# Optimization experiments

Hardware: AMD Instinct MI355X
Metric: run time of the kernel (lower is better)

## Reference

```python
import jax, jax.numpy as jnp
import numpy as np

N_NODES = 100000
N_EDGES = 1600000


def _gcn_conv(x, src, dst, W, b, n_nodes):
    """PyG GCNConv: add self-loops, symmetric norm, linear, scatter-add."""
    h = x @ W  # [N, out]
    # append self-loops
    loop = jnp.arange(n_nodes, dtype=src.dtype)
    s = jnp.concatenate([src, loop])
    d = jnp.concatenate([dst, loop])
    # degree over destinations (with self-loops)
    deg = jax.ops.segment_sum(jnp.ones_like(d, dtype=h.dtype), d, num_segments=n_nodes)
    dinv = jax.lax.rsqrt(jnp.maximum(deg, 1.0))
    norm = dinv[s] * dinv[d]  # [E+N]
    msg = h[s] * norm[:, None]  # [E+N, out] gather + scale
    out = jax.ops.segment_sum(msg, d, num_segments=n_nodes)  # scatter-add
    return out + b


def setup_inputs() -> dict:
    key = jax.random.key(0)
    k1, k2, k3, k4 = jax.random.split(key, 4)
    x = jax.random.normal(k1, (N_NODES, 10), dtype=jnp.float32)
    edge_index = jax.random.randint(k2, (2, N_EDGES), 0, N_NODES, dtype=jnp.int64)
    W1 = jax.random.normal(k3, (10, 64), dtype=jnp.float32) * (1.0 / np.sqrt(10))
    b1 = jnp.zeros((64,), dtype=jnp.float32)
    W2 = jax.random.normal(k4, (64, 10), dtype=jnp.float32) * (1.0 / np.sqrt(64))
    b2 = jnp.zeros((10,), dtype=jnp.float32)
    return {"x": x, "edge_index": edge_index, "W1": W1, "b1": b1, "W2": W2, "b2": b2}


def reference(x, edge_index, W1, b1, W2, b2):
    src, dst = edge_index[0], edge_index[1]
    h = _gcn_conv(x, src, dst, W1, b1, N_NODES)
    h = jax.nn.relu(h)
    # dropout is identity in eval mode
    h = _gcn_conv(h, src, dst, W2, b2, N_NODES)
    return jax.nn.log_softmax(h, axis=1)
```

## Files before the change

### kernel.cpp

```cpp
#include <hip/hip_runtime.h>
#include <hip/hip_fp16.h>

#define N_NODES 100000
#define N_EDGES 1600000

#define NPB   256
#define NB    391
#define PCAP  8192
#define ABLK  256
#define ATHR  1024
#define CAP   64

typedef unsigned int u32;

__device__ __forceinline__ float2 h2f2(u32 u) {
    __half2 h = *reinterpret_cast<__half2*>(&u);
    return __half22float2(h);
}

__global__ void zero_tail_kernel(int* __restrict__ tail) {
    tail[threadIdx.x] = 0;
}

__global__ __launch_bounds__(ATHR) void bucket_kernel(
    const int* __restrict__ src, const int* __restrict__ dst,
    int* __restrict__ tail, int* __restrict__ pairs, int E) {
    __shared__ int lcnt[NB];
    __shared__ int bbase[NB];
    const int tid = threadIdx.x;
    for (int b = tid; b < NB; b += ATHR) lcnt[b] = 0;
    __syncthreads();

    const int chunk = (E + gridDim.x - 1) / gridDim.x;
    const int e0 = blockIdx.x * chunk;
    const int e1 = min(e0 + chunk, E);

    for (int e = e0 + tid; e < e1; e += ATHR)
        atomicAdd(&lcnt[dst[e] >> 8], 1);
    __syncthreads();

    for (int b = tid; b < NB; b += ATHR) {
        int n = lcnt[b];
        int ng8 = (n + 7) & ~7;
        int base = 0;
        if (ng8) {
            base = atomicAdd(&tail[b], ng8);
            if (base + ng8 <= PCAP) {
                for (int j = n; j < ng8; ++j) pairs[b * PCAP + base + j] = -1;
            }
        }
        bbase[b] = base;
        lcnt[b] = 0;
    }
    __syncthreads();

    for (int e = e0 + tid; e < e1; e += ATHR) {
        int d = dst[e];
        int b = d >> 8;
        int p = (src[e] << 8) | (d & 255);
        int pos = atomicAdd(&lcnt[b], 1);
        int idx = bbase[b] + pos;
        if (idx < PCAP) pairs[b * PCAP + idx] = p;
    }
}

__global__ __launch_bounds__(1024) void csr_kernel(
    const int* __restrict__ tail, const int* __restrict__ pairs,
    const float* __restrict__ x, int* __restrict__ cnt, int* __restrict__ slist,
    float* __restrict__ dinv, u32* __restrict__ xh, u32* __restrict__ th, int N) {
    __shared__ int ofs[NPB];
    const int b = blockIdx.x, tid = threadIdx.x;
    if (tid < NPB) ofs[tid] = 0;
    __syncthreads();
    const int n = min(tail[b], PCAP);
    const int* pb = pairs + b * PCAP;
    const int node0 = b * NPB;
    for (int i = tid; i < n; i += 1024) {
        int p = pb[i];
        if (p >= 0) {
            int dl = p & 255;
            int pos = atomicAdd(&ofs[dl], 1);
            if (pos < CAP) slist[(size_t)(node0 + dl) * CAP + pos] = p >> 8;
        }
    }
    __syncthreads();
    if (tid < NPB) {
        int node = node0 + tid;
        if (node < N) {
            int deg = min(ofs[tid], CAP);
            cnt[node] = deg;
            int padded = (deg + 3) & ~3;
            for (int j = deg; j < padded; ++j) slist[(size_t)node * CAP + j] = N_NODES;
            float di = rsqrtf((float)deg + 1.0f);
            dinv[node] = di;
            u32 h[8];
#pragma unroll
            for (int k = 0; k < 5; ++k) {
                __half2 hh = __floats2half2_rn(x[(size_t)node * 10 + 2 * k] * di,
                                               x[(size_t)node * 10 + 2 * k + 1] * di);
                h[k] = *reinterpret_cast<u32*>(&hh);
            }
            h[5] = h[6] = h[7] = 0u;
            u32* row = xh + (size_t)node * 8;
            ((uint4*)row)[0] = make_uint4(h[0], h[1], h[2], h[3]);
            ((uint4*)row)[1] = make_uint4(h[4], h[5], h[6], h[7]);
        }
    }
    if (b == 0 && tid == 0) {
        u32* rx = xh + (size_t)N * 8;
        u32* rt = th + (size_t)N * 8;
        ((uint4*)rx)[0] = make_uint4(0, 0, 0, 0); ((uint4*)rx)[1] = make_uint4(0, 0, 0, 0);
        ((uint4*)rt)[0] = make_uint4(0, 0, 0, 0); ((uint4*)rt)[1] = make_uint4(0, 0, 0, 0);
    }
}

__global__ void aggh_kernel(const u32* __restrict__ vh, const int* __restrict__ cnt,
                            const int* __restrict__ slist, float* __restrict__ out12, int N) {
    int gt = blockIdx.x * blockDim.x + threadIdx.x;
    int i = gt >> 1, cg = gt & 1;
    if (i >= N) return;
    int degi = cnt[i];
    const int* lst = slist + (size_t)i * CAP;
    float a[8];
    {
        uint4 s = *(((const uint4*)(vh + (size_t)i * 8)) + cg);
        float2 f0 = h2f2(s.x), f1 = h2f2(s.y), f2 = h2f2(s.z), f3 = h2f2(s.w);
        a[0] = f0.x; a[1] = f0.y; a[2] = f1.x; a[3] = f1.y;
        a[4] = f2.x; a[5] = f2.y; a[6] = f3.x; a[7] = f3.y;
    }
    for (int k = 0; k < degi; k += 4) {
        int4 s4 = *reinterpret_cast<const int4*>(lst + k);
        uint4 q0 = *(((const uint4*)(vh + (size_t)s4.x * 8)) + cg);
        uint4 q1 = *(((const uint4*)(vh + (size_t)s4.y * 8)) + cg);
        uint4 q2 = *(((const uint4*)(vh + (size_t)s4.z * 8)) + cg);
        uint4 q3 = *(((const uint4*)(vh + (size_t)s4.w * 8)) + cg);
        float2 f;
        f = h2f2(q0.x); a[0] += f.x; a[1] += f.y;  f = h2f2(q0.y); a[2] += f.x; a[3] += f.y;
        f = h2f2(q0.z); a[4] += f.x; a[5] += f.y;  f = h2f2(q0.w); a[6] += f.x; a[7] += f.y;
        f = h2f2(q1.x); a[0] += f.x; a[1] += f.y;  f = h2f2(q1.y); a[2] += f.x; a[3] += f.y;
        f = h2f2(q1.z); a[4] += f.x; a[5] += f.y;  f = h2f2(q1.w); a[6] += f.x; a[7] += f.y;
        f = h2f2(q2.x); a[0] += f.x; a[1] += f.y;  f = h2f2(q2.y); a[2] += f.x; a[3] += f.y;
        f = h2f2(q2.z); a[4] += f.x; a[5] += f.y;  f = h2f2(q2.w); a[6] += f.x; a[7] += f.y;
        f = h2f2(q3.x); a[0] += f.x; a[1] += f.y;  f = h2f2(q3.y); a[2] += f.x; a[3] += f.y;
        f = h2f2(q3.z); a[4] += f.x; a[5] += f.y;  f = h2f2(q3.w); a[6] += f.x; a[7] += f.y;
    }
    float* orow = out12 + (size_t)i * 12;
    if (cg == 0) {
        ((float4*)orow)[0] = make_float4(a[0], a[1], a[2], a[3]);
        ((float4*)orow)[1] = make_float4(a[4], a[5], a[6], a[7]);
    } else {
        *(float2*)(orow + 8) = make_float2(a[0], a[1]);
    }
}

__global__ void layer12_kernel(const float* __restrict__ agg12, const float* __restrict__ dinv,
                               const float* __restrict__ W1, const float* __restrict__ b1,
                               const float* __restrict__ W2, u32* __restrict__ th, int N) {
    __shared__ float sW1[640];
    __shared__ float sW2[640];
    __shared__ float sb1[64];
    for (int k = threadIdx.x; k < 640; k += blockDim.x) { sW1[k] = W1[k]; sW2[k] = W2[k]; }
    if (threadIdx.x < 64) sb1[threadIdx.x] = b1[threadIdx.x];
    __syncthreads();
    int i = blockIdx.x * blockDim.x + threadIdx.x;
    if (i >= N) return;
    float di = dinv[i];
    float ax[10];
#pragma unroll
    for (int k = 0; k < 10; ++k) ax[k] = di * agg12[(size_t)i * 12 + k];
    float o[10];
#pragma unroll
    for (int k = 0; k < 10; ++k) o[k] = 0.f;
    for (int c = 0; c < 64; ++c) {
        float y = sb1[c];
#pragma unroll
        for (int k = 0; k < 10; ++k) y = fmaf(ax[k], sW1[k * 64 + c], y);
        y = fmaxf(y, 0.f);
#pragma unroll
        for (int k = 0; k < 10; ++k) o[k] = fmaf(y, sW2[c * 10 + k], o[k]);
    }
    u32 h[8];
#pragma unroll
    for (int k = 0; k < 5; ++k) {
        __half2 hh = __floats2half2_rn(o[2 * k] * di, o[2 * k + 1] * di);
        h[k] = *reinterpret_cast<u32*>(&hh);
    }
    h[5] = h[6] = h[7] = 0u;
    u32* row = th + (size_t)i * 8;
    ((uint4*)row)[0] = make_uint4(h[0], h[1], h[2], h[3]);
    ((uint4*)row)[1] = make_uint4(h[4], h[5], h[6], h[7]);
}

__global__ void aggout_kernel(const u32* __restrict__ vh, const int* __restrict__ cnt,
                              const int* __restrict__ slist, const float* __restrict__ dinv,
                              const float* __restrict__ b2, float* __restrict__ out, int N) {
    int gt = blockIdx.x * blockDim.x + threadIdx.x;
    int i = gt >> 1, cg = gt & 1;
    bool valid = (i < N);
    float a[8];
#pragma unroll
    for (int k = 0; k < 8; ++k) a[k] = 0.f;
    if (valid) {
        int degi = cnt[i];
        const int* lst = slist + (size_t)i * CAP;
        {
            uint4 s = *(((const uint4*)(vh + (size_t)i * 8)) + cg);
            float2 f0 = h2f2(s.x), f1 = h2f2(s.y), f2 = h2f2(s.z), f3 = h2f2(s.w);
            a[0] = f0.x; a[1] = f0.y; a[2] = f1.x; a[3] = f1.y;
            a[4] = f2.x; a[5] = f2.y; a[6] = f3.x; a[7] = f3.y;
        }
        for (int k = 0; k < degi; k += 4) {
            int4 s4 = *reinterpret_cast<const int4*>(lst + k);
            uint4 q0 = *(((const uint4*)(vh + (size_t)s4.x * 8)) + cg);
            uint4 q1 = *(((const uint4*)(vh + (size_t)s4.y * 8)) + cg);
            uint4 q2 = *(((const uint4*)(vh + (size_t)s4.z * 8)) + cg);
            uint4 q3 = *(((const uint4*)(vh + (size_t)s4.w * 8)) + cg);
            float2 f;
            f = h2f2(q0.x); a[0] += f.x; a[1] += f.y;  f = h2f2(q0.y); a[2] += f.x; a[3] += f.y;
            f = h2f2(q0.z); a[4] += f.x; a[5] += f.y;  f = h2f2(q0.w); a[6] += f.x; a[7] += f.y;
            f = h2f2(q1.x); a[0] += f.x; a[1] += f.y;  f = h2f2(q1.y); a[2] += f.x; a[3] += f.y;
            f = h2f2(q1.z); a[4] += f.x; a[5] += f.y;  f = h2f2(q1.w); a[6] += f.x; a[7] += f.y;
            f = h2f2(q2.x); a[0] += f.x; a[1] += f.y;  f = h2f2(q2.y); a[2] += f.x; a[3] += f.y;
            f = h2f2(q2.z); a[4] += f.x; a[5] += f.y;  f = h2f2(q2.w); a[6] += f.x; a[7] += f.y;
            f = h2f2(q3.x); a[0] += f.x; a[1] += f.y;  f = h2f2(q3.y); a[2] += f.x; a[3] += f.y;
            f = h2f2(q3.z); a[4] += f.x; a[5] += f.y;  f = h2f2(q3.w); a[6] += f.x; a[7] += f.y;
        }
    }
    float v8 = __shfl_xor(a[0], 1);
    float v9 = __shfl_xor(a[1], 1);
    if (valid && cg == 0) {
        float di = dinv[i];
        float v[10] = { a[0], a[1], a[2], a[3], a[4], a[5], a[6], a[7], v8, v9 };
        float m = -1e30f;
#pragma unroll
        for (int c = 0; c < 10; ++c) {
            v[c] = fmaf(di, v[c], b2[c]);
            m = fmaxf(m, v[c]);
        }
        float s = 0.f;
#pragma unroll
        for (int c = 0; c < 10; ++c) s += __expf(v[c] - m);
        float lse = __logf(s) + m;
        float2* po = (float2*)(out + (size_t)i * 10);
#pragma unroll
        for (int c = 0; c < 5; ++c) po[c] = make_float2(v[2 * c] - lse, v[2 * c + 1] - lse);
    }
}

extern "C" void kernel_launch(void* const* d_in, const int* in_sizes, int n_in,
                              void* d_out, int out_size, void* d_ws, size_t ws_size,
                              hipStream_t stream) {
    const float* x  = (const float*)d_in[0];
    const int*   ei = (const int*)d_in[1];
    const float* W1 = (const float*)d_in[2];
    const float* b1 = (const float*)d_in[3];
    const float* W2 = (const float*)d_in[4];
    const float* b2 = (const float*)d_in[5];
    float* out = (float*)d_out;

    const int N = N_NODES, E = N_EDGES;
    const int* src = ei;
    const int* dst = ei + E;

    int*   tail  = (int*)d_ws;
    int*   pairs = tail + 512;
    int*   cnt   = pairs + (size_t)NB * PCAP;
    int*   slist = cnt + N;
    float* dinv  = (float*)(slist + (size_t)N * CAP);
    u32*   xh    = (u32*)(dinv + N);
    u32*   th    = xh + (size_t)(N + 1) * 8;
    float* agg12 = (float*)(th + (size_t)(N + 1) * 8);

    zero_tail_kernel<<<1, 512, 0, stream>>>(tail);
    bucket_kernel<<<ABLK, ATHR, 0, stream>>>(src, dst, tail, pairs, E);
    csr_kernel<<<NB, 1024, 0, stream>>>(tail, pairs, x, cnt, slist, dinv, xh, th, N);
    aggh_kernel<<<(2 * N + 255) / 256, 256, 0, stream>>>(xh, cnt, slist, agg12, N);
    layer12_kernel<<<(N + 255) / 256, 256, 0, stream>>>(agg12, dinv, W1, b1, W2, th, N);
    aggout_kernel<<<(2 * N + 255) / 256, 256, 0, stream>>>(th, cnt, slist, dinv, b2, out, N);
}
```

Baseline: 93.27 us.

## Use per-block fixed bucket slots and fuse aggregation with MLP layer

The bucketing pass now writes edges into fixed per-(bucket, block) slots with a count table. This removes the global tail atomics, the zeroing kernel and the second counting pass over the edge list. The first aggregation is fused with the dense two-layer MLP: the two threads per node exchange partial sums via shuffles and each computes half of the 64 hidden channels, which avoids the agg12 round-trip and one launch. The cost is that the CSR kernel now scans a fixed 256x64 slot grid per bucket. Slots are capped at 64 edges per block and bucket, so overflow would silently drop edges.

```diff
diff --git a/kernel.cpp b/kernel.cpp
--- a/kernel.cpp
+++ b/kernel.cpp
@@ -6,9 +6,9 @@
 
 #define NPB   256
 #define NB    391
-#define PCAP  8192
 #define ABLK  256
 #define ATHR  1024
+#define BSLOT 64
 #define CAP   64
 
 typedef unsigned int u32;
@@ -18,66 +18,47 @@
     return __half22float2(h);
 }
 
-__global__ void zero_tail_kernel(int* __restrict__ tail) {
-    tail[threadIdx.x] = 0;
-}
-
 __global__ __launch_bounds__(ATHR) void bucket_kernel(
     const int* __restrict__ src, const int* __restrict__ dst,
-    int* __restrict__ tail, int* __restrict__ pairs, int E) {
+    int* __restrict__ gcnt, int* __restrict__ pairs, int E) {
     __shared__ int lcnt[NB];
-    __shared__ int bbase[NB];
-    const int tid = threadIdx.x;
+    const int tid = threadIdx.x, blk = blockIdx.x;
     for (int b = tid; b < NB; b += ATHR) lcnt[b] = 0;
     __syncthreads();
 
     const int chunk = (E + gridDim.x - 1) / gridDim.x;
-    const int e0 = blockIdx.x * chunk;
+    const int e0 = blk * chunk;
     const int e1 = min(e0 + chunk, E);
-
-    for (int e = e0 + tid; e < e1; e += ATHR)
-        atomicAdd(&lcnt[dst[e] >> 8], 1);
-    __syncthreads();
-
-    for (int b = tid; b < NB; b += ATHR) {
-        int n = lcnt[b];
-        int ng8 = (n + 7) & ~7;
-        int base = 0;
-        if (ng8) {
-            base = atomicAdd(&tail[b], ng8);
-            if (base + ng8 <= PCAP) {
-                for (int j = n; j < ng8; ++j) pairs[b * PCAP + base + j] = -1;
-            }
-        }
-        bbase[b] = base;
-        lcnt[b] = 0;
-    }
-    __syncthreads();
 
     for (int e = e0 + tid; e < e1; e += ATHR) {
         int d = dst[e];
         int b = d >> 8;
         int p = (src[e] << 8) | (d & 255);
         int pos = atomicAdd(&lcnt[b], 1);
-        int idx = bbase[b] + pos;
-        if (idx < PCAP) pairs[b * PCAP + idx] = p;
-    }
+        if (pos < BSLOT) pairs[(size_t)b * (ABLK * BSLOT) + blk * BSLOT + pos] = p;
+    }
+    __syncthreads();
+    for (int b = tid; b < NB; b += ATHR)
+        gcnt[b * ABLK + blk] = min(lcnt[b], BSLOT);
 }
 
 __global__ __launch_bounds__(1024) void csr_kernel(
-    const int* __restrict__ tail, const int* __restrict__ pairs,
+    const int* __restrict__ gcnt, const int* __restrict__ pairs,
     const float* __restrict__ x, int* __restrict__ cnt, int* __restrict__ slist,
     float* __restrict__ dinv, u32* __restrict__ xh, u32* __restrict__ th, int N) {
     __shared__ int ofs[NPB];
+    __shared__ int gc[ABLK];
     const int b = blockIdx.x, tid = threadIdx.x;
     if (tid < NPB) ofs[tid] = 0;
-    __syncthreads();
-    const int n = min(tail[b], PCAP);
-    const int* pb = pairs + b * PCAP;
+    if (tid < ABLK) gc[tid] = gcnt[b * ABLK + tid];
+    __syncthreads();
+    const int* pb = pairs + (size_t)b * (ABLK * BSLOT);
     const int node0 = b * NPB;
-    for (int i = tid; i < n; i += 1024) {
-        int p = pb[i];
-        if (p >= 0) {
+    for (int i = tid; i < ABLK * BSLOT; i += 1024) {
+        int r = i >> 6;
+        int j = i & 63;
+        if (j < gc[r]) {
+            int p = pb[i];
             int dl = p & 255;
             int pos = atomicAdd(&ofs[dl], 1);
             if (pos < CAP) slist[(size_t)(node0 + dl) * CAP + pos] = p >> 8;
@@ -114,8 +95,16 @@
     }
 }
 
-__global__ void aggh_kernel(const u32* __restrict__ vh, const int* __restrict__ cnt,
-                            const int* __restrict__ slist, float* __restrict__ out12, int N) {
+__global__ void aggmlp_kernel(const u32* __restrict__ vh, const int* __restrict__ cnt,
+                              const int* __restrict__ slist, const float* __restrict__ dinv,
+                              const float* __restrict__ W1, const float* __restrict__ b1,
+                              const float* __restrict__ W2, u32* __restrict__ th, int N) {
+    __shared__ float sW1[640];
+    __shared__ float sW2[640];
+    __shared__ float sb1[64];
+    for (int k = threadIdx.x; k < 640; k += blockDim.x) { sW1[k] = W1[k]; sW2[k] = W2[k]; }
+    if (threadIdx.x < 64) sb1[threadIdx.x] = b1[threadIdx.x];
+    __syncthreads();
     int gt = blockIdx.x * blockDim.x + threadIdx.x;
     int i = gt >> 1, cg = gt & 1;
     if (i >= N) return;
@@ -144,34 +133,26 @@
         f = h2f2(q3.x); a[0] += f.x; a[1] += f.y;  f = h2f2(q3.y); a[2] += f.x; a[3] += f.y;
         f = h2f2(q3.z); a[4] += f.x; a[5] += f.y;  f = h2f2(q3.w); a[6] += f.x; a[7] += f.y;
     }
-    float* orow = out12 + (size_t)i * 12;
-    if (cg == 0) {
-        ((float4*)orow)[0] = make_float4(a[0], a[1], a[2], a[3]);
-        ((float4*)orow)[1] = make_float4(a[4], a[5], a[6], a[7]);
-    } else {
-        *(float2*)(orow + 8) = make_float2(a[0], a[1]);
-    }
-}
-
-__global__ void layer12_kernel(const float* __restrict__ agg12, const float* __restrict__ dinv,
-                               const float* __restrict__ W1, const float* __restrict__ b1,
-                               const float* __restrict__ W2, u32* __restrict__ th, int N) {
-    __shared__ float sW1[640];
-    __shared__ float sW2[640];
-    __shared__ float sb1[64];
-    for (int k = threadIdx.x; k < 640; k += blockDim.x) { sW1[k] = W1[k]; sW2[k] = W2[k]; }
-    if (threadIdx.x < 64) sb1[threadIdx.x] = b1[threadIdx.x];
-    __syncthreads();
-    int i = blockIdx.x * blockDim.x + threadIdx.x;
-    if (i >= N) return;
+    float t0 = __shfl_xor(a[0], 1), t1 = __shfl_xor(a[1], 1);
+    float t2 = __shfl_xor(a[2], 1), t3 = __shfl_xor(a[3], 1);
+    float t4 = __shfl_xor(a[4], 1), t5 = __shfl_xor(a[5], 1);
+    float t6 = __shfl_xor(a[6], 1), t7 = __shfl_xor(a[7], 1);
     float di = dinv[i];
     float ax[10];
-#pragma unroll
-    for (int k = 0; k < 10; ++k) ax[k] = di * agg12[(size_t)i * 12 + k];
+    if (cg == 0) {
+        ax[0]=a[0]; ax[1]=a[1]; ax[2]=a[2]; ax[3]=a[3]; ax[4]=a[4];
+        ax[5]=a[5]; ax[6]=a[6]; ax[7]=a[7]; ax[8]=t0;   ax[9]=t1;
+    } else {
+        ax[0]=t0; ax[1]=t1; ax[2]=t2; ax[3]=t3; ax[4]=t4;
+        ax[5]=t5; ax[6]=t6; ax[7]=t7; ax[8]=a[0]; ax[9]=a[1];
+    }
+#pragma unroll
+    for (int k = 0; k < 10; ++k) ax[k] *= di;
     float o[10];
 #pragma unroll
     for (int k = 0; k < 10; ++k) o[k] = 0.f;
-    for (int c = 0; c < 64; ++c) {
+    const int c0 = cg * 32;
+    for (int c = c0; c < c0 + 32; ++c) {
         float y = sb1[c];
 #pragma unroll
         for (int k = 0; k < 10; ++k) y = fmaf(ax[k], sW1[k * 64 + c], y);
@@ -179,16 +160,22 @@
 #pragma unroll
         for (int k = 0; k < 10; ++k) o[k] = fmaf(y, sW2[c * 10 + k], o[k]);
     }
-    u32 h[8];
-#pragma unroll
-    for (int k = 0; k < 5; ++k) {
-        __half2 hh = __floats2half2_rn(o[2 * k] * di, o[2 * k + 1] * di);
-        h[k] = *reinterpret_cast<u32*>(&hh);
-    }
-    h[5] = h[6] = h[7] = 0u;
+#pragma unroll
+    for (int k = 0; k < 10; ++k) o[k] += __shfl_xor(o[k], 1);
+#pragma unroll
+    for (int k = 0; k < 10; ++k) o[k] *= di;
     u32* row = th + (size_t)i * 8;
-    ((uint4*)row)[0] = make_uint4(h[0], h[1], h[2], h[3]);
-    ((uint4*)row)[1] = make_uint4(h[4], h[5], h[6], h[7]);
+    if (cg == 0) {
+        __half2 h0 = __floats2half2_rn(o[0], o[1]);
+        __half2 h1 = __floats2half2_rn(o[2], o[3]);
+        __half2 h2 = __floats2half2_rn(o[4], o[5]);
+        __half2 h3 = __floats2half2_rn(o[6], o[7]);
+        ((uint4*)row)[0] = make_uint4(*reinterpret_cast<u32*>(&h0), *reinterpret_cast<u32*>(&h1),
+                                      *reinterpret_cast<u32*>(&h2), *reinterpret_cast<u32*>(&h3));
+    } else {
+        __half2 h4 = __floats2half2_rn(o[8], o[9]);
+        ((uint4*)row)[1] = make_uint4(*reinterpret_cast<u32*>(&h4), 0u, 0u, 0u);
+    }
 }
 
 __global__ void aggout_kernel(const u32* __restrict__ vh, const int* __restrict__ cnt,
@@ -262,19 +249,16 @@
     const int* src = ei;
     const int* dst = ei + E;
 
-    int*   tail  = (int*)d_ws;
-    int*   pairs = tail + 512;
-    int*   cnt   = pairs + (size_t)NB * PCAP;
+    int*   gcnt  = (int*)d_ws;
+    int*   pairs = gcnt + (size_t)NB * ABLK;
+    int*   cnt   = pairs + (size_t)NB * ABLK * BSLOT;
     int*   slist = cnt + N;
     float* dinv  = (float*)(slist + (size_t)N * CAP);
     u32*   xh    = (u32*)(dinv + N);
     u32*   th    = xh + (size_t)(N + 1) * 8;
-    float* agg12 = (float*)(th + (size_t)(N + 1) * 8);
-
-    zero_tail_kernel<<<1, 512, 0, stream>>>(tail);
-    bucket_kernel<<<ABLK, ATHR, 0, stream>>>(src, dst, tail, pairs, E);
-    csr_kernel<<<NB, 1024, 0, stream>>>(tail, pairs, x, cnt, slist, dinv, xh, th, N);
-    aggh_kernel<<<(2 * N + 255) / 256, 256, 0, stream>>>(xh, cnt, slist, agg12, N);
-    layer12_kernel<<<(N + 255) / 256, 256, 0, stream>>>(agg12, dinv, W1, b1, W2, th, N);
+
+    bucket_kernel<<<ABLK, ATHR, 0, stream>>>(src, dst, gcnt, pairs, E);
+    csr_kernel<<<NB, 1024, 0, stream>>>(gcnt, pairs, x, cnt, slist, dinv, xh, th, N);
+    aggmlp_kernel<<<(2 * N + 255) / 256, 256, 0, stream>>>(xh, cnt, slist, dinv, W1, b1, W2, th, N);
     aggout_kernel<<<(2 * N + 255) / 256, 256, 0, stream>>>(th, cnt, slist, dinv, b2, out, N);
 }
```

After: 83.17 us. 10.8% less time.
